# Optimization experiments

Measured on AMD Instinct MI355X. Metric: run time of the kernel, lower is better.

Reference implementation:

```python
import jax, jax.numpy as jnp
import numpy as np

B = 16; Hp = 24; Wp = 24; N = Hp * Wp + 2  # 578 = patches + cls + freq tokens
D = 768; H = 12; HDIM = D // H
BAND = 64; SD = 16  # sd = min(16, max(4, band_dim))
HID = 3072  # int(embed_dim * mlp_ratio)
SCALE = HDIM ** -0.5; CLIP = 10.0
FILM_SCALE = 0.5; SPEC_INIT = 0.02; GATE_INIT = 0.05


def _ln(x, w, b, eps=1e-6):
    m = jnp.mean(x, axis=-1, keepdims=True)
    v = jnp.mean((x - m) ** 2, axis=-1, keepdims=True)
    return (x - m) * jax.lax.rsqrt(v + eps) * w + b


def _rms(x, eps=1e-6):
    return x * jax.lax.rsqrt(jnp.mean(x * x, axis=-1, keepdims=True) + eps)


def setup_inputs() -> dict:
    key = jax.random.key(0)
    ks = jax.random.split(key, 16)
    rn = lambda k, s, sc=1.0: jax.random.normal(k, s, dtype=jnp.float32) * sc
    return {
        "x": rn(ks[0], (B, N, D)),
        "band_tokens": rn(ks[1], (B, 1, D)),  # unused by forward (matches torch signature)
        "freq_token_for_cond": rn(ks[2], (B, 1, D)),
        "freq_summary": rn(ks[3], (B, D)),
        "token_band_feat": rn(ks[4], (B, N, BAND)),
        "alpha": jnp.ones((1,), jnp.float32),
        "ln_gate_w": jnp.ones((D,), jnp.float32), "ln_gate_b": jnp.zeros((D,), jnp.float32),
        "film_w": rn(ks[5], (D, 2 * D), 1e-4), "film_b": jnp.zeros((2 * D,), jnp.float32),
        "ln_attn_w": jnp.ones((D,), jnp.float32), "ln_attn_b": jnp.zeros((D,), jnp.float32),
        "qkv_w": rn(ks[6], (D, 3 * D), 0.02), "qkv_b": jnp.zeros((3 * D,), jnp.float32),
        "proj_w": rn(ks[7], (D, D), 0.02), "proj_b": jnp.zeros((D,), jnp.float32),
        "spec_bias_scale": jnp.float32(SPEC_INIT),
        "gate_w": rn(ks[8], (D, H), 1e-4), "gate_b": jnp.zeros((H,), jnp.float32),
        "band_proj_w": rn(ks[9], (BAND, SD), 0.02),
        "ln_mlp_w": jnp.ones((D,), jnp.float32), "ln_mlp_b": jnp.zeros((D,), jnp.float32),
        "fc1_w": rn(ks[10], (D, HID), 0.02), "fc1_b": jnp.zeros((HID,), jnp.float32),
        "fc2_w": rn(ks[11], (HID, D), 0.02), "fc2_b": jnp.zeros((D,), jnp.float32),
        "dw_w": rn(ks[12], (HID, 1, 3, 3), 0.1), "dw_b": jnp.zeros((HID,), jnp.float32),
    }


def _forward(x, band_tokens, freq_token_for_cond, freq_summary, token_band_feat, alpha,
             ln_gate_w, ln_gate_b, film_w, film_b, ln_attn_w, ln_attn_b,
             qkv_w, qkv_b, proj_w, proj_b, spec_bias_scale, gate_w, gate_b, band_proj_w,
             ln_mlp_w, ln_mlp_b, fc1_w, fc1_b, fc2_w, fc2_b, dw_w, dw_b):
    a = alpha.reshape(())
    # --- FiLM gate on patch tokens (replaces patch, no residual) ---
    cls_freq = x[:, :2]
    patch = x[:, 2:]
    p = _ln(patch, ln_gate_w, ln_gate_b)
    gb = freq_summary @ film_w + film_b            # [B, 2D]
    gamma, beta = jnp.split(gb, 2, axis=-1)
    gamma = jnp.tanh(gamma) * FILM_SCALE
    beta = jnp.tanh(beta) * FILM_SCALE
    patch = p * (1.0 + a * gamma[:, None, :]) + a * beta[:, None, :]
    x = jnp.concatenate([cls_freq, patch], axis=1)
    # --- spectral-similarity attention ---
    xn = _ln(x, ln_attn_w, ln_attn_b)
    qkv = (xn @ qkv_w + qkv_b).reshape(B, N, 3, H, HDIM)
    q = _rms(qkv[:, :, 0].transpose(0, 2, 1, 3))   # [B,H,N,hd]
    k = _rms(qkv[:, :, 1].transpose(0, 2, 1, 3))
    v = qkv[:, :, 2].transpose(0, 2, 1, 3)
    logits = jnp.einsum('bhnd,bhmd->bhnm', q * SCALE, k)
    s = _rms(token_band_feat @ band_proj_w)        # [B,N,SD]
    ssim = jnp.einsum('bns,bms->bnm', s, s)        # [B,N,N]
    logits = jnp.clip(logits + a * spec_bias_scale * ssim[:, None], -CLIP, CLIP)
    attn = jax.nn.softmax(logits, axis=-1)
    out = jnp.einsum('bhnm,bhmd->bhnd', attn, v)
    g = jnp.tanh(freq_token_for_cond[:, 0] @ gate_w + gate_b) * GATE_INIT  # [B,H]
    out = out * (1.0 + a * g[:, :, None, None])
    out = out.transpose(0, 2, 1, 3).reshape(B, N, D)
    x = x + (out @ proj_w + proj_b)
    # --- conv MLP on patch tokens only ---
    cls_freq = x[:, :2]
    patch = x[:, 2:]
    h = jax.nn.gelu(_ln(patch, ln_mlp_w, ln_mlp_b) @ fc1_w + fc1_b, approximate=False)
    h = h.transpose(0, 2, 1).reshape(B, HID, Hp, Wp)
    h = jax.lax.conv_general_dilated(h, dw_w, (1, 1), 'SAME', feature_group_count=HID,
                                     dimension_numbers=('NCHW', 'OIHW', 'NCHW'))
    h = jax.nn.silu(h + dw_b[None, :, None, None])
    h = h.reshape(B, HID, Hp * Wp).transpose(0, 2, 1)
    patch = patch + (h @ fc2_w + fc2_b)
    return jnp.concatenate([cls_freq, patch], axis=1)


def reference(x, band_tokens, freq_token_for_cond, freq_summary, token_band_feat, alpha,
              ln_gate_w, ln_gate_b, film_w, film_b, ln_attn_w, ln_attn_b,
              qkv_w, qkv_b, proj_w, proj_b, spec_bias_scale, gate_w, gate_b, band_proj_w,
              ln_mlp_w, ln_mlp_b, fc1_w, fc1_b, fc2_w, fc2_b, dw_w, dw_b):
    return _forward(x, band_tokens, freq_token_for_cond, freq_summary, token_band_feat, alpha,
                    ln_gate_w, ln_gate_b, film_w, film_b, ln_attn_w, ln_attn_b,
                    qkv_w, qkv_b, proj_w, proj_b, spec_bias_scale, gate_w, gate_b, band_proj_w,
                    ln_mlp_w, ln_mlp_b, fc1_w, fc1_b, fc2_w, fc2_b, dw_w, dw_b)
```

## Files before the change

### kernel.cpp

```cpp
#include <hip/hip_runtime.h>
#include <hip/hip_bf16.h>

#define BATCH 16
#define NTOK 578
#define NTOKP 592
#define NP 576
#define PGRID 24
#define DIM 768
#define NH 12
#define HDIM 64
#define BAND 64
#define SDIM 16
#define HID 3072
#define SCALE 0.125f
#define CLIPV 10.0f
#define KHS 104
#define VTS 72
#define PLS 72

typedef __attribute__((ext_vector_type(8))) short bf16x8;
typedef __attribute__((ext_vector_type(4))) float f32x4;

__device__ __forceinline__ float b2f(short u) {
  union { float f; unsigned int i; } x;
  x.i = ((unsigned int)(unsigned short)u) << 16;
  return x.f;
}
__device__ __forceinline__ short f2b(float x) {
  __hip_bfloat16 h = __float2bfloat16(x);
  return *reinterpret_cast<short*>(&h);
}

__device__ __forceinline__ void gload16(const short* g, short* l) {
  __builtin_amdgcn_global_load_lds(
      (const __attribute__((address_space(1))) unsigned int*)g,
      (__attribute__((address_space(3))) unsigned int*)l, 16, 0, 0);
}

__device__ __forceinline__ int swz_wgid(int orig, int nwg) {
  int xcd = orig & 7, i = orig >> 3;
  int q = nwg >> 3, r = nwg & 7;
  return (xcd < r) ? xcd * (q + 1) + i : r * (q + 1) + (xcd - r) * q + i;
}

__device__ __forceinline__ void block_reduce2(float& a, float& b) {
  __shared__ float sm[8];
  #pragma unroll
  for (int o = 32; o > 0; o >>= 1) { a += __shfl_down(a, o); b += __shfl_down(b, o); }
  int lane = threadIdx.x & 63, w = threadIdx.x >> 6;
  __syncthreads();
  if (lane == 0) { sm[w] = a; sm[4 + w] = b; }
  __syncthreads();
  a = sm[0] + sm[1] + sm[2] + sm[3];
  b = sm[4] + sm[5] + sm[6] + sm[7];
}

__device__ __forceinline__ void tw_body(
    const float* __restrict__ W, short* __restrict__ Wt, int K, int N,
    int kblk, int nblk, float (*t)[33]) {
  int k0 = kblk * 32, n0 = nblk * 32;
  int tx = threadIdx.x & 31, ty = threadIdx.x >> 5;
  #pragma unroll
  for (int i = 0; i < 4; i++)
    t[ty + 8 * i][tx] = W[(size_t)(k0 + ty + 8 * i) * N + n0 + tx];
  __syncthreads();
  #pragma unroll
  for (int i = 0; i < 4; i++)
    Wt[(size_t)(n0 + ty + 8 * i) * K + k0 + tx] = f2b(t[tx][ty + 8 * i]);
}

__global__ __launch_bounds__(256) void prep_weights(
    const float* __restrict__ qkv_w, const float* __restrict__ proj_w,
    const float* __restrict__ fc1_w, const float* __restrict__ fc2_w,
    const float* __restrict__ dww,
    short* __restrict__ qkvT, short* __restrict__ projT,
    short* __restrict__ fc1T, short* __restrict__ fc2T, float* __restrict__ dwt) {
  __shared__ float t[32][33];
  int id = blockIdx.x;
  if (id < 1728) {
    tw_body(qkv_w, qkvT, 768, 2304, id % 24, id / 24, t);
  } else if (id < 2304) {
    int u = id - 1728; tw_body(proj_w, projT, 768, 768, u % 24, u / 24, t);
  } else if (id < 4608) {
    int u = id - 2304; tw_body(fc1_w, fc1T, 768, 3072, u % 24, u / 24, t);
  } else if (id < 6912) {
    int u = id - 4608; tw_body(fc2_w, fc2T, 3072, 768, u % 96, u / 96, t);
  } else {
    int i = (id - 6912) * 256 + threadIdx.x;
    if (i < 9 * HID) { int tt = i / HID, c = i - tt * HID; dwt[i] = dww[c * 9 + tt]; }
  }
}

__global__ __launch_bounds__(256) void transpose_v(
    const short* __restrict__ v, short* __restrict__ vT) {
  __shared__ short t[64][72];
  int bh = blockIdx.y;
  int n0 = blockIdx.x * 64;
  int tid = threadIdx.x;
  const short* vb = v + (size_t)bh * NTOK * HDIM;
  short* ob = vT + (size_t)bh * HDIM * NTOKP;
  {
    int r = tid >> 2, c0 = (tid & 3) * 16;
    int n = n0 + r;
    bf16x8 a0 = {0,0,0,0,0,0,0,0}, a1 = {0,0,0,0,0,0,0,0};
    if (n < NTOK) {
      a0 = *(const bf16x8*)(vb + (size_t)n * HDIM + c0);
      a1 = *(const bf16x8*)(vb + (size_t)n * HDIM + c0 + 8);
    }
    *(bf16x8*)(&t[r][c0]) = a0;
    *(bf16x8*)(&t[r][c0 + 8]) = a1;
  }
  __syncthreads();
  {
    int d = tid & 63, nc = tid >> 6;
    int nbase = n0 + nc * 16;
    short tmp[16];
    #pragma unroll
    for (int e = 0; e < 16; e++) tmp[e] = t[nc * 16 + e][d];
    if (nbase + 16 <= NTOK) {
      *(bf16x8*)(ob + (size_t)d * NTOKP + nbase) = *(bf16x8*)tmp;
      *(bf16x8*)(ob + (size_t)d * NTOKP + nbase + 8) = *(bf16x8*)(tmp + 8);
    } else {
      for (int e = 0; e < 16; e++)
        if (nbase + e < NTOK) ob[(size_t)d * NTOKP + nbase + e] = tmp[e];
    }
  }
}

__global__ __launch_bounds__(256) void film_kernel(
    const float* __restrict__ fsum, const float* __restrict__ film_w, const float* __restrict__ film_b,
    const float* __restrict__ ftc, const float* __restrict__ gate_w, const float* __restrict__ gate_b,
    float* __restrict__ gamma, float* __restrict__ beta, float* __restrict__ g) {
  int bid = blockIdx.x, tid = threadIdx.x;
  if (bid < 24) {
    __shared__ float fs[BATCH][DIM];
    for (int i = tid; i < BATCH * DIM; i += 256) fs[i / DIM][i - (i / DIM) * DIM] = fsum[i];
    __syncthreads();
    int col = bid * 64 + (tid & 63);
    int b0 = tid >> 6;
    float acc[4];
    float bv = film_b[col];
    #pragma unroll
    for (int i = 0; i < 4; i++) acc[i] = bv;
    for (int k = 0; k < DIM; k++) {
      float w = film_w[(size_t)k * 2 * DIM + col];
      #pragma unroll
      for (int i = 0; i < 4; i++) acc[i] += fs[b0 + 4 * i][k] * w;
    }
    #pragma unroll
    for (int i = 0; i < 4; i++) {
      int b = b0 + 4 * i;
      float t = tanhf(acc[i]) * 0.5f;
      if (col < DIM) gamma[b * DIM + col] = t;
      else beta[b * DIM + (col - DIM)] = t;
    }
  } else {
    int i2 = tid;
    if (i2 < BATCH * NH) {
      int b = i2 / NH, h = i2 - b * NH;
      float acc = gate_b[h];
      for (int i = 0; i < DIM; i++) acc += ftc[b * DIM + i] * gate_w[i * NH + h];
      g[i2] = tanhf(acc) * 0.05f;
    }
  }
}

__global__ __launch_bounds__(256) void ln_film_kernel(
    const float* __restrict__ x, const float* __restrict__ gamma, const float* __restrict__ beta,
    const float* __restrict__ gw, const float* __restrict__ gb,
    const float* __restrict__ aw, const float* __restrict__ ab,
    const float* __restrict__ alpha, float* __restrict__ xw, __hip_bfloat16* __restrict__ xn) {
  int row = blockIdx.x;
  int b = row / NTOK, n = row % NTOK;
  int tid = threadIdx.x;
  const float* xr = x + (size_t)row * DIM;
  float vals[3];
  #pragma unroll
  for (int j = 0; j < 3; j++) vals[j] = xr[tid + j * 256];
  if (n >= 2) {
    float s = vals[0] + vals[1] + vals[2];
    float ss = vals[0]*vals[0] + vals[1]*vals[1] + vals[2]*vals[2];
    block_reduce2(s, ss);
    float mean = s * (1.f / 768.f);
    float inv = rsqrtf(ss * (1.f / 768.f) - mean * mean + 1e-6f);
    float a = alpha[0];
    #pragma unroll
    for (int j = 0; j < 3; j++) {
      int d = tid + j * 256;
      float p = (vals[j] - mean) * inv * gw[d] + gb[d];
      vals[j] = p * (1.f + a * gamma[(size_t)b * DIM + d]) + a * beta[(size_t)b * DIM + d];
    }
  }
  float* xwr = xw + (size_t)row * DIM;
  #pragma unroll
  for (int j = 0; j < 3; j++) xwr[tid + j * 256] = vals[j];
  float s = vals[0] + vals[1] + vals[2];
  float ss = vals[0]*vals[0] + vals[1]*vals[1] + vals[2]*vals[2];
  block_reduce2(s, ss);
  float mean = s * (1.f / 768.f);
  float inv = rsqrtf(ss * (1.f / 768.f) - mean * mean + 1e-6f);
  __hip_bfloat16* xnr = xn + (size_t)row * DIM;
  #pragma unroll
  for (int j = 0; j < 3; j++) {
    int d = tid + j * 256;
    xnr[d] = __float2bfloat16((vals[j] - mean) * inv * aw[d] + ab[d]);
  }
}

__global__ __launch_bounds__(256) void band_s_kernel(
    const float* __restrict__ tbf, const float* __restrict__ bw, float* __restrict__ s) {
  int row = blockIdx.x * 4 + (threadIdx.x >> 6);
  int lane = threadIdx.x & 63;
  if (row >= BATCH * NTOK) return;
  const float* t = tbf + (size_t)row * BAND;
  float val = 0.f;
  if (lane < SDIM) {
    for (int i = 0; i < BAND; i++) val += t[i] * bw[i * SDIM + lane];
  }
  float ss = val * val;
  #pragma unroll
  for (int o = 8; o > 0; o >>= 1) ss += __shfl_xor(ss, o, 16);
  if (lane < SDIM) s[(size_t)row * SDIM + lane] = val * rsqrtf(ss * (1.f / 16.f) + 1e-6f);
}

__device__ __forceinline__ void stage_tile256(
    const short* __restrict__ A, const short* __restrict__ Wt, int K,
    int m0, int n0, int kt, short* Al, short* Bl, int wid, int lrow, int lcol) {
  #pragma unroll
  for (int it = 0; it < 4; it++) {
    int r0 = wid * 8 + it * 64;
    gload16(A + (size_t)(m0 + r0 + lrow) * K + kt + lcol, Al + r0 * 64);
  }
  #pragma unroll
  for (int it = 0; it < 2; it++) {
    int r0 = wid * 8 + it * 64;
    gload16(Wt + (size_t)(n0 + r0 + lrow) * K + kt + lcol, Bl + r0 * 64);
  }
}

__device__ __forceinline__ void compute_tile256(
    const short* Al, const short* Bl, f32x4 acc[4][4],
    int wr, int wc, int ln15, int kb) {
  #pragma unroll
  for (int kk = 0; kk < 2; kk++) {
    bf16x8 af[4], bfr[4];
    #pragma unroll
    for (int i = 0; i < 4; i++)
      af[i] = *(const bf16x8*)(Al + (wr * 64 + i * 16 + ln15) * 64 + kk * 32 + kb * 8);
    #pragma unroll
    for (int j = 0; j < 4; j++)
      bfr[j] = *(const bf16x8*)(Bl + (wc * 64 + j * 16 + ln15) * 64 + kk * 32 + kb * 8);
    #pragma unroll
    for (int i = 0; i < 4; i++)
      #pragma unroll
      for (int j = 0; j < 4; j++)
        acc[i][j] = __builtin_amdgcn_mfma_f32_16x16x32_bf16(af[i], bfr[j], acc[i][j], 0, 0, 0);
  }
}

__device__ __forceinline__ void mfma_core_256(
    const short* __restrict__ A, const short* __restrict__ Wt,
    int K, int m0, int n0, f32x4 acc[4][4], short* Al, short* Bl) {
  int tid = threadIdx.x, lane = tid & 63, wid = tid >> 6;
  int wr = wid >> 1, wc = wid & 1;
  int ln15 = lane & 15, kb = lane >> 4;
  int lrow = lane >> 3, lcol = (lane & 7) * 8;
  #pragma unroll
  for (int i = 0; i < 4; i++)
    #pragma unroll
    for (int j = 0; j < 4; j++) acc[i][j] = (f32x4){0.f, 0.f, 0.f, 0.f};
  for (int kt = 0; kt < K; kt += 64) {
    stage_tile256(A, Wt, K, m0, n0, kt, Al, Bl, wid, lrow, lcol);
    __syncthreads();
    compute_tile256(Al, Bl, acc, wr, wc, ln15, kb);
    __syncthreads();
  }
}

__device__ __forceinline__ void stage_tile(
    const short* __restrict__ A, const short* __restrict__ Wt, int K,
    int m0, int n0, int kt, short* Al, short* Bl, int wid, int lrow, int lcol) {
  #pragma unroll
  for (int it = 0; it < 4; it++) {
    int r0 = wid * 8 + it * 32;
    gload16(A + (size_t)(m0 + r0 + lrow) * K + kt + lcol, Al + r0 * 64);
    gload16(Wt + (size_t)(n0 + r0 + lrow) * K + kt + lcol, Bl + r0 * 64);
  }
}

__device__ __forceinline__ void stage_tile64(
    const short* __restrict__ A, const short* __restrict__ Wt, int K,
    int m0, int n0, int kt, short* Al, short* Bl, int wid, int lrow, int lcol) {
  #pragma unroll
  for (int it = 0; it < 2; it++) {
    int r0 = wid * 8 + it * 32;
    gload16(A + (size_t)(m0 + r0 + lrow) * K + kt + lcol, Al + r0 * 64);
  }
  #pragma unroll
  for (int it = 0; it < 4; it++) {
    int r0 = wid * 8 + it * 32;
    gload16(Wt + (size_t)(n0 + r0 + lrow) * K + kt + lcol, Bl + r0 * 64);
  }
}

__device__ __forceinline__ void compute_tile64(
    const short* Al, const short* Bl, f32x4 acc[4][2],
    int wid, int ln15, int kb) {
  #pragma unroll
  for (int kk = 0; kk < 2; kk++) {
    bf16x8 af[4], bfr[2];
    #pragma unroll
    for (int i = 0; i < 4; i++)
      af[i] = *(const bf16x8*)(Al + (i * 16 + ln15) * 64 + kk * 32 + kb * 8);
    #pragma unroll
    for (int j = 0; j < 2; j++)
      bfr[j] = *(const bf16x8*)(Bl + (wid * 32 + j * 16 + ln15) * 64 + kk * 32 + kb * 8);
    #pragma unroll
    for (int i = 0; i < 4; i++)
      #pragma unroll
      for (int j = 0; j < 2; j++)
        acc[i][j] = __builtin_amdgcn_mfma_f32_16x16x32_bf16(af[i], bfr[j], acc[i][j], 0, 0, 0);
  }
}

__device__ __forceinline__ void mfma_core_64(
    const short* __restrict__ A, const short* __restrict__ Wt,
    int K, int m0, int n0, f32x4 acc[4][2],
    short* Al0, short* Bl0, short* Al1, short* Bl1) {
  int tid = threadIdx.x, lane = tid & 63, wid = tid >> 6;
  int ln15 = lane & 15, kb = lane >> 4;
  int lrow = lane >> 3, lcol = (lane & 7) * 8;
  #pragma unroll
  for (int i = 0; i < 4; i++)
    #pragma unroll
    for (int j = 0; j < 2; j++) acc[i][j] = (f32x4){0.f, 0.f, 0.f, 0.f};
  stage_tile64(A, Wt, K, m0, n0, 0, Al0, Bl0, wid, lrow, lcol);
  __syncthreads();
  for (int kt = 0; kt < K; kt += 128) {
    if (kt + 64 < K)
      stage_tile64(A, Wt, K, m0, n0, kt + 64, Al1, Bl1, wid, lrow, lcol);
    compute_tile64(Al0, Bl0, acc, wid, ln15, kb);
    __syncthreads();
    if (kt + 128 < K)
      stage_tile64(A, Wt, K, m0, n0, kt + 128, Al0, Bl0, wid, lrow, lcol);
    if (kt + 64 < K)
      compute_tile64(Al1, Bl1, acc, wid, ln15, kb);
    __syncthreads();
  }
}

__global__ __launch_bounds__(512) void gemm_qkv(
    const short* __restrict__ A, const short* __restrict__ Wt, const float* __restrict__ bias,
    __hip_bfloat16* __restrict__ q, __hip_bfloat16* __restrict__ k, __hip_bfloat16* __restrict__ v) {
  __shared__ short Al[256 * 64], Bl[128 * 64];
  f32x4 acc[4][4];
  int wgid = swz_wgid(blockIdx.x, 37 * 18);
  int m0 = (wgid / 18) * 256, n0 = (wgid % 18) * 128;
  mfma_core_256(A, Wt, DIM, m0, n0, acc, Al, Bl);
  int tid = threadIdx.x, lane = tid & 63, wid = tid >> 6, wr = wid >> 1, wc = wid & 1;
  int ln15 = lane & 15, lq = lane >> 4;
  int colbase = n0 + wc * 64;
  int which = colbase / DIM;
  int rem = colbase - which * DIM;
  int h = rem >> 6;
  __hip_bfloat16* dst = (which == 0) ? q : ((which == 1) ? k : v);
  float fin_scale = (which == 0) ? SCALE : 1.0f;
  float bv[4];
  #pragma unroll
  for (int j = 0; j < 4; j++) bv[j] = bias[colbase + j * 16 + ln15];
  #pragma unroll
  for (int i = 0; i < 4; i++) {
    #pragma unroll
    for (int r = 0; r < 4; r++) {
      int m = m0 + wr * 64 + i * 16 + lq * 4 + r;
      float v4[4];
      #pragma unroll
      for (int j = 0; j < 4; j++) v4[j] = acc[i][j][r] + bv[j];
      float inv = fin_scale;
      if (which < 2) {
        float ss = v4[0]*v4[0] + v4[1]*v4[1] + v4[2]*v4[2] + v4[3]*v4[3];
        ss += __shfl_xor(ss, 1); ss += __shfl_xor(ss, 2);
        ss += __shfl_xor(ss, 4); ss += __shfl_xor(ss, 8);
        inv = rsqrtf(ss * (1.f / 64.f) + 1e-6f) * fin_scale;
      }
      if (m < BATCH * NTOK) {
        int b = m / NTOK, n = m - b * NTOK;
        __hip_bfloat16* orow = dst + (((size_t)b * NH + h) * NTOK + n) * HDIM;
        #pragma unroll
        for (int j = 0; j < 4; j++)
          orow[j * 16 + ln15] = __float2bfloat16(v4[j] * inv);
      }
    }
  }
}

__global__ __launch_bounds__(512) void attn_mfma(
    const short* __restrict__ q, const short* __restrict__ k,
    const short* __restrict__ vT, const float* __restrict__ s,
    const float* __restrict__ g, const float* __restrict__ alpha,
    const float* __restrict__ sbs, short* __restrict__ ao) {
  __shared__ short Kh[2][64 * KHS];
  __shared__ short Vt[2][64 * VTS];
  __shared__ short Pl[8][16 * PLS];
  int xcd = blockIdx.x & 7, idx = blockIdx.x >> 3;
  int bh = xcd * 24 + idx / 5;
  int n0 = (idx % 5) * 128;
  int b = bh / NH, h = bh - b * NH;
  int tid = threadIdx.x, lane = tid & 63, w = tid >> 6;
  int l15 = lane & 15, lg = lane >> 4;
  float a = alpha[0], c = a * sbs[0];
  const short* qb = q + (size_t)bh * NTOK * HDIM;
  const short* kb = k + (size_t)bh * NTOK * HDIM;
  const short* vtb = vT + (size_t)bh * HDIM * NTOKP;
  const float* sb = s + (size_t)b * NTOK * SDIM;
  const bf16x8 Z8 = {0, 0, 0, 0, 0, 0, 0, 0};

  int qrow = n0 + w * 16 + l15;
  int qsrc = (qrow < NTOK) ? qrow : 0;
  bf16x8 qf0 = *(const bf16x8*)(qb + (size_t)qsrc * HDIM + lg * 8);
  bf16x8 qf1 = *(const bf16x8*)(qb + (size_t)qsrc * HDIM + 32 + lg * 8);
  bf16x8 qf2 = Z8;
  if (lg < 2) {
    const float* sp = sb + (size_t)qsrc * SDIM + lg * 8;
    #pragma unroll
    for (int j = 0; j < 8; j++) qf2[j] = f2b(c * sp[j]);
  }

  f32x4 accO[4];
  #pragma unroll
  for (int dd = 0; dd < 4; dd++) accO[dd] = (f32x4){0.f, 0.f, 0.f, 0.f};
  float rsum[4] = {0.f, 0.f, 0.f, 0.f};

  int srow = (tid & 255) >> 2, sseg = tid & 3;
  if (tid < 256 && sseg == 3) {
    #pragma unroll
    for (int bb = 0; bb < 2; bb++) {
      short* dst = Kh[bb] + srow * KHS + 80;
      *(bf16x8*)dst = Z8;
      *(bf16x8*)(dst + 8) = Z8;
    }
  }

  auto stage = [&](int mt, short* KhB, short* VtB) {
// ... 58 lines not shown
      sa[jj] = __builtin_amdgcn_mfma_f32_16x16x32_bf16(qf2, *(const bf16x8*)(kp + 64), sa[jj], 0, 0, 0);
    }
    __builtin_amdgcn_s_setprio(0);
    short* pw = Pl[w];
    float ps[4][4];
    #pragma unroll
    for (int jj = 0; jj < 4; jj++) {
      bool ok = (mt + jj * 16 + l15) < NTOK;
      #pragma unroll
      for (int r = 0; r < 4; r++) {
        float x = sa[jj][r];
        x = fminf(fmaxf(x, -CLIPV), CLIPV);
        float e = ok ? __expf(x) : 0.f;
        ps[jj][r] = e;
        pw[(lg * 4 + r) * PLS + jj * 16 + l15] = f2b(e);
      }
    }
    #pragma unroll
    for (int r = 0; r < 4; r++) {
      float t = ps[0][r] + ps[1][r] + ps[2][r] + ps[3][r];
      t += __shfl_xor(t, 1); t += __shfl_xor(t, 2);
      t += __shfl_xor(t, 4); t += __shfl_xor(t, 8);
      rsum[r] += t;
    }
    __builtin_amdgcn_s_setprio(1);
    #pragma unroll
    for (int kc = 0; kc < 2; kc++) {
      bf16x8 pa = *(const bf16x8*)(pw + l15 * PLS + kc * 32 + lg * 8);
      #pragma unroll
      for (int dd = 0; dd < 4; dd++) {
        bf16x8 vf = *(const bf16x8*)(VtC + (dd * 16 + l15) * VTS + kc * 32 + lg * 8);
        accO[dd] = __builtin_amdgcn_mfma_f32_16x16x32_bf16(pa, vf, accO[dd], 0, 0, 0);
      }
    }
    __builtin_amdgcn_s_setprio(0);
    __syncthreads();
  }
  float gm = 1.f + a * g[bh];
  #pragma unroll
  for (int r = 0; r < 4; r++) {
    int n = n0 + w * 16 + lg * 4 + r;
    if (n >= NTOK) continue;
    float inv = gm / rsum[r];
    short* orow = ao + ((size_t)b * NTOK + n) * DIM + h * HDIM;
    #pragma unroll
    for (int dd = 0; dd < 4; dd++)
      orow[dd * 16 + l15] = f2b(accO[dd][r] * inv);
  }
}

__global__ __launch_bounds__(256) void gemm_proj(
    const short* __restrict__ A, const short* __restrict__ Wt, const float* __restrict__ bias,
    float* __restrict__ xw, float* __restrict__ out) {
  __shared__ short Al[2 * 64 * 64], Bl[2 * 128 * 64];
  f32x4 acc[4][2];
  int wgid = swz_wgid(blockIdx.x, 145 * 6);
  int m0 = (wgid / 6) * 64, n0 = (wgid % 6) * 128;
  mfma_core_64(A, Wt, DIM, m0, n0, acc, Al, Bl, Al + 64 * 64, Bl + 128 * 64);
  int tid = threadIdx.x, lane = tid & 63, wid = tid >> 6;
  int ln15 = lane & 15, lq = lane >> 4;
  #pragma unroll
  for (int i = 0; i < 4; i++) {
    #pragma unroll
    for (int j = 0; j < 2; j++) {
      int col = n0 + wid * 32 + j * 16 + ln15;
      float bv = bias[col];
      #pragma unroll
      for (int r = 0; r < 4; r++) {
        int m = m0 + i * 16 + lq * 4 + r;
        if (m >= BATCH * NTOK) continue;
        int n = m % NTOK;
        float val = acc[i][j][r] + bv + xw[(size_t)m * DIM + col];
        xw[(size_t)m * DIM + col] = val;
        if (n < 2) out[(size_t)m * DIM + col] = val;
      }
    }
  }
}

__global__ __launch_bounds__(256) void ln_mlp_kernel(
    const float* __restrict__ x2, const float* __restrict__ w, const float* __restrict__ bb,
    __hip_bfloat16* __restrict__ xm) {
  int r = blockIdx.x;
  int b = r / NP, pi = r % NP;
  int tid = threadIdx.x;
  const float* xr = x2 + ((size_t)b * NTOK + 2 + pi) * DIM;
  float vals[3];
  #pragma unroll
  for (int j = 0; j < 3; j++) vals[j] = xr[tid + j * 256];
  float s = vals[0] + vals[1] + vals[2];
  float ss = vals[0]*vals[0] + vals[1]*vals[1] + vals[2]*vals[2];
  block_reduce2(s, ss);
  float mean = s * (1.f / 768.f);
  float inv = rsqrtf(ss * (1.f / 768.f) - mean * mean + 1e-6f);
  __hip_bfloat16* xo = xm + (size_t)r * DIM;
  #pragma unroll
  for (int j = 0; j < 3; j++) {
    int d = tid + j * 256;
    xo[d] = __float2bfloat16((vals[j] - mean) * inv * w[d] + bb[d]);
  }
}

__global__ __launch_bounds__(512) void gemm_fc1(
    const short* __restrict__ A, const short* __restrict__ Wt, const float* __restrict__ bias,
    __hip_bfloat16* __restrict__ h1) {
  __shared__ short Al[256 * 64], Bl[128 * 64];
  f32x4 acc[4][4];
  int wgid = swz_wgid(blockIdx.x, 18 * 24);
  int m0 = (wgid / 24) * 256, n0 = (wgid % 24) * 128;
  mfma_core_256(A, Wt, DIM, m0, n0, acc, Al, Bl);
  int tid = threadIdx.x, lane = tid & 63, wid = tid >> 6, wr = wid >> 1, wc = wid & 1;
  int ln15 = lane & 15, lq = lane >> 4;
  #pragma unroll
  for (int i = 0; i < 4; i++) {
    #pragma unroll
    for (int j = 0; j < 4; j++) {
      int col = n0 + wc * 64 + j * 16 + ln15;
      float bv = bias[col];
      #pragma unroll
      for (int r = 0; r < 4; r++) {
        int m = m0 + wr * 64 + i * 16 + lq * 4 + r;
        float val = acc[i][j][r] + bv;
        float ge = 0.5f * val * (1.f + erff(val * 0.70710678118f));
        h1[(size_t)m * HID + col] = __float2bfloat16(ge);
      }
    }
  }
}

__global__ __launch_bounds__(256) void dwconv_kernel(
    const __hip_bfloat16* __restrict__ h1, const float* __restrict__ dwt,
    const float* __restrict__ dwb, __hip_bfloat16* __restrict__ h2) {
  int gx = blockIdx.x;
  int b = gx / 144, g = gx - b * 144;
  int y = g / 6, x0 = (g - y * 6) * 4;
  int tid = threadIdx.x;
  int c0 = blockIdx.y * 512 + (tid & 63) * 8;
  int x = x0 + (tid >> 6);
  const short* in = (const short*)h1 + (size_t)b * NP * HID + c0;
  bf16x8 iv[3][3];
  #pragma unroll
  for (int ky = 0; ky < 3; ky++) {
    int yy = y + ky - 1;
    #pragma unroll
    for (int kx = 0; kx < 3; kx++) {
      int xx = x + kx - 1;
      bool ok = (yy >= 0 && yy < PGRID && xx >= 0 && xx < PGRID);
      iv[ky][kx] = ok ? *(const bf16x8*)(in + (size_t)(yy * PGRID + xx) * HID)
                      : (bf16x8){0, 0, 0, 0, 0, 0, 0, 0};
    }
  }
  float acc[8];
  {
    float4 b0 = *(const float4*)(dwb + c0);
    float4 b1 = *(const float4*)(dwb + c0 + 4);
    acc[0] = b0.x; acc[1] = b0.y; acc[2] = b0.z; acc[3] = b0.w;
    acc[4] = b1.x; acc[5] = b1.y; acc[6] = b1.z; acc[7] = b1.w;
  }
  #pragma unroll
  for (int t = 0; t < 9; t++) {
    float4 w0 = *(const float4*)(dwt + t * HID + c0);
    float4 w1 = *(const float4*)(dwt + t * HID + c0 + 4);
    bf16x8 xv = iv[t / 3][t % 3];
    acc[0] += b2f(xv[0]) * w0.x; acc[1] += b2f(xv[1]) * w0.y;
    acc[2] += b2f(xv[2]) * w0.z; acc[3] += b2f(xv[3]) * w0.w;
    acc[4] += b2f(xv[4]) * w1.x; acc[5] += b2f(xv[5]) * w1.y;
    acc[6] += b2f(xv[6]) * w1.z; acc[7] += b2f(xv[7]) * w1.w;
  }
  short ov[8];
  #pragma unroll
  for (int e = 0; e < 8; e++) {
    float v = acc[e];
    ov[e] = f2b(v / (1.f + __expf(-v)));
  }
  *(bf16x8*)((short*)h2 + ((size_t)b * NP + y * PGRID + x) * HID + c0) = *(bf16x8*)ov;
}

__global__ __launch_bounds__(256) void gemm_fc2(
    const short* __restrict__ A, const short* __restrict__ Wt, const float* __restrict__ bias,
    const float* __restrict__ xw, float* __restrict__ out, int b0) {
  __shared__ short Al[2 * 64 * 64], Bl[2 * 128 * 64];
  f32x4 acc[4][2];
  int wgid = swz_wgid(blockIdx.x, 72 * 6);
  int m0 = (wgid / 6) * 64, n0 = (wgid % 6) * 128;
  mfma_core_64(A, Wt, HID, m0, n0, acc, Al, Bl, Al + 64 * 64, Bl + 128 * 64);
  int tid = threadIdx.x, lane = tid & 63, wid = tid >> 6;
  int ln15 = lane & 15, lq = lane >> 4;
  #pragma unroll
  for (int i = 0; i < 4; i++) {
    #pragma unroll
    for (int j = 0; j < 2; j++) {
      int col = n0 + wid * 32 + j * 16 + ln15;
      float bv = bias[col];
      #pragma unroll
      for (int r = 0; r < 4; r++) {
        int m = m0 + i * 16 + lq * 4 + r;
        int bl = m / NP, pi = m - bl * NP;
        size_t orow = ((size_t)(b0 + bl) * NTOK + 2 + pi) * DIM;
        out[orow + col] = acc[i][j][r] + bv + xw[orow + col];
      }
    }
  }
}

extern "C" void kernel_launch(void* const* d_in, const int* in_sizes, int n_in,
                              void* d_out, int out_size, void* d_ws, size_t ws_size,
                              hipStream_t stream) {
  const float* x      = (const float*)d_in[0];
  const float* ftc    = (const float*)d_in[2];
  const float* fsum   = (const float*)d_in[3];
  const float* tbf    = (const float*)d_in[4];
  const float* alpha  = (const float*)d_in[5];
  const float* lgw    = (const float*)d_in[6];
  const float* lgb    = (const float*)d_in[7];
  const float* film_w = (const float*)d_in[8];
  const float* film_b = (const float*)d_in[9];
  const float* law    = (const float*)d_in[10];
  const float* lab    = (const float*)d_in[11];
  const float* qkv_w  = (const float*)d_in[12];
  const float* qkv_b  = (const float*)d_in[13];
  const float* proj_w = (const float*)d_in[14];
  const float* proj_b = (const float*)d_in[15];
  const float* sbs    = (const float*)d_in[16];
  const float* gate_w = (const float*)d_in[17];
  const float* gate_b = (const float*)d_in[18];
  const float* band_w = (const float*)d_in[19];
  const float* lmw    = (const float*)d_in[20];
  const float* lmb    = (const float*)d_in[21];
  const float* fc1_w  = (const float*)d_in[22];
  const float* fc1_b  = (const float*)d_in[23];
  const float* fc2_w  = (const float*)d_in[24];
  const float* fc2_b  = (const float*)d_in[25];
  const float* dw_w   = (const float*)d_in[26];
  const float* dw_b   = (const float*)d_in[27];
  float* out = (float*)d_out;

  float* ws = (float*)d_ws;
  const size_t SZ = (size_t)BATCH * NTOK * DIM;

  float* p_xw = ws;
  short* p_xn = (short*)(ws + SZ);
  short* p_q  = (short*)(ws + SZ + SZ / 2);
  short* p_k  = (short*)(ws + 2 * SZ);
  short* p_v  = (short*)(ws + 2 * SZ + SZ / 2);
  float* p_s  = ws + 3 * SZ;
  float* p_gamma = p_s + (size_t)BATCH * NTOK * SDIM;
  float* p_beta  = p_gamma + BATCH * DIM;
  float* p_g     = p_beta + BATCH * DIM;
  float* p_dwt   = p_g + 256;
  float* wtb = p_dwt + 9 * HID;
  short* qkvT = (short*)wtb;
  short* projT = qkvT + (size_t)768 * 2304;
  short* fc1T  = projT + (size_t)768 * 768;
  short* fc2T  = fc1T + (size_t)768 * 3072;
  short* h2c   = fc2T + (size_t)3072 * 768;

  const size_t total_floats =
      3 * SZ + (size_t)BATCH * NTOK * SDIM + 2 * (size_t)BATCH * DIM + 256 + 9 * HID +
      ((size_t)768 * 2304 + 768 * 768 + 768 * 3072 + 3072 * 768) / 2 +
      ((size_t)8 * NP * HID) / 2;
  if (ws_size < total_floats * sizeof(float)) return;

  short* p_ao = p_xn;
  short* p_xm = p_q;
  short* h1c  = p_k;
  short* p_vT = h2c;

  dim3 blk(256);

  prep_weights<<<dim3(7020), blk, 0, stream>>>(
      qkv_w, proj_w, fc1_w, fc2_w, dw_w, qkvT, projT, fc1T, fc2T, p_dwt);

  film_kernel<<<dim3(25), blk, 0, stream>>>(
      fsum, film_w, film_b, ftc, gate_w, gate_b, p_gamma, p_beta, p_g);

  ln_film_kernel<<<dim3(BATCH * NTOK), blk, 0, stream>>>(
      x, p_gamma, p_beta, lgw, lgb, law, lab, alpha, p_xw, (__hip_bfloat16*)p_xn);

  band_s_kernel<<<dim3((BATCH * NTOK + 3) / 4), blk, 0, stream>>>(tbf, band_w, p_s);

  gemm_qkv<<<dim3(37 * 18), dim3(512), 0, stream>>>(
      p_xn, qkvT, qkv_b, (__hip_bfloat16*)p_q, (__hip_bfloat16*)p_k, (__hip_bfloat16*)p_v);

  transpose_v<<<dim3(10, BATCH * NH), blk, 0, stream>>>(p_v, p_vT);

  attn_mfma<<<dim3(960), dim3(512), 0, stream>>>(
      p_q, p_k, p_vT, p_s, p_g, alpha, sbs, p_ao);

  gemm_proj<<<dim3(145 * 6), blk, 0, stream>>>(p_ao, projT, proj_b, p_xw, out);

  ln_mlp_kernel<<<dim3(BATCH * NP), blk, 0, stream>>>(p_xw, lmw, lmb, (__hip_bfloat16*)p_xm);

  for (int cc = 0; cc < 2; cc++) {
    const short* Ach = p_xm + (size_t)cc * 4608 * DIM;
    gemm_fc1<<<dim3(18 * 24), dim3(512), 0, stream>>>(Ach, fc1T, fc1_b, (__hip_bfloat16*)h1c);
    dwconv_kernel<<<dim3(8 * 144, 6), blk, 0, stream>>>(
        (const __hip_bfloat16*)h1c, p_dwt, dw_b, (__hip_bfloat16*)h2c);
    gemm_fc2<<<dim3(72 * 6), blk, 0, stream>>>(h2c, fc2T, fc2_b, p_xw, out, cc * 8);
  }
}
```

Before: 517.3 us.

## Double-buffer GEMM LDS staging and write V transposed from QKV GEMM

Replaces the single-buffered and ping-pong GEMM main loops with a two-stage prefetch pipeline. The loop uses explicit vmcnt waits and raw s_barrier, so global loads for tile t+2 overlap the MFMA work on tile t. The QKV GEMM epilogue now writes V directly into the transposed vT layout, which removes the separate transpose kernel and its extra round trip through memory. In exchange, LDS use for the 256-row GEMMs doubles, which may lower occupancy. The vT stores are strided single-element writes that may coalesce poorly.

```diff
diff --git a/kernel.cpp b/kernel.cpp
--- a/kernel.cpp
+++ b/kernel.cpp
@@ -91,42 +91,6 @@
   }
 }
 
-__global__ __launch_bounds__(256) void transpose_v(
-    const short* __restrict__ v, short* __restrict__ vT) {
-  __shared__ short t[64][72];
-  int bh = blockIdx.y;
-  int n0 = blockIdx.x * 64;
-  int tid = threadIdx.x;
-  const short* vb = v + (size_t)bh * NTOK * HDIM;
-  short* ob = vT + (size_t)bh * HDIM * NTOKP;
-  {
-    int r = tid >> 2, c0 = (tid & 3) * 16;
-    int n = n0 + r;
-    bf16x8 a0 = {0,0,0,0,0,0,0,0}, a1 = {0,0,0,0,0,0,0,0};
-    if (n < NTOK) {
-      a0 = *(const bf16x8*)(vb + (size_t)n * HDIM + c0);
-      a1 = *(const bf16x8*)(vb + (size_t)n * HDIM + c0 + 8);
-    }
-    *(bf16x8*)(&t[r][c0]) = a0;
-    *(bf16x8*)(&t[r][c0 + 8]) = a1;
-  }
-  __syncthreads();
-  {
-    int d = tid & 63, nc = tid >> 6;
-    int nbase = n0 + nc * 16;
-    short tmp[16];
-    #pragma unroll
-    for (int e = 0; e < 16; e++) tmp[e] = t[nc * 16 + e][d];
-    if (nbase + 16 <= NTOK) {
-      *(bf16x8*)(ob + (size_t)d * NTOKP + nbase) = *(bf16x8*)tmp;
-      *(bf16x8*)(ob + (size_t)d * NTOKP + nbase + 8) = *(bf16x8*)(tmp + 8);
-    } else {
-      for (int e = 0; e < 16; e++)
-        if (nbase + e < NTOK) ob[(size_t)d * NTOKP + nbase + e] = tmp[e];
-    }
-  }
-}
-
 __global__ __launch_bounds__(256) void film_kernel(
     const float* __restrict__ fsum, const float* __restrict__ film_w, const float* __restrict__ film_b,
     const float* __restrict__ ftc, const float* __restrict__ gate_w, const float* __restrict__ gate_b,
@@ -223,7 +187,7 @@
   if (lane < SDIM) s[(size_t)row * SDIM + lane] = val * rsqrtf(ss * (1.f / 16.f) + 1e-6f);
 }
 
-__device__ __forceinline__ void stage_tile256(
+__device__ __forceinline__ void stage256(
     const short* __restrict__ A, const short* __restrict__ Wt, int K,
     int m0, int n0, int kt, short* Al, short* Bl, int wid, int lrow, int lcol) {
   #pragma unroll
@@ -238,7 +202,7 @@
   }
 }
 
-__device__ __forceinline__ void compute_tile256(
+__device__ __forceinline__ void compute256(
     const short* Al, const short* Bl, f32x4 acc[4][4],
     int wr, int wc, int ln15, int kb) {
   #pragma unroll
@@ -258,9 +222,10 @@
   }
 }
 
-__device__ __forceinline__ void mfma_core_256(
+__device__ __forceinline__ void core256c(
     const short* __restrict__ A, const short* __restrict__ Wt,
-    int K, int m0, int n0, f32x4 acc[4][4], short* Al, short* Bl) {
+    int K, int m0, int n0, f32x4 acc[4][4],
+    short* Al0, short* Bl0, short* Al1, short* Bl1) {
   int tid = threadIdx.x, lane = tid & 63, wid = tid >> 6;
   int wr = wid >> 1, wc = wid & 1;
   int ln15 = lane & 15, kb = lane >> 4;
@@ -269,26 +234,29 @@
   for (int i = 0; i < 4; i++)
     #pragma unroll
     for (int j = 0; j < 4; j++) acc[i][j] = (f32x4){0.f, 0.f, 0.f, 0.f};
-  for (int kt = 0; kt < K; kt += 64) {
-    stage_tile256(A, Wt, K, m0, n0, kt, Al, Bl, wid, lrow, lcol);
-    __syncthreads();
-    compute_tile256(Al, Bl, acc, wr, wc, ln15, kb);
-    __syncthreads();
-  }
-}
-
-__device__ __forceinline__ void stage_tile(
-    const short* __restrict__ A, const short* __restrict__ Wt, int K,
-    int m0, int n0, int kt, short* Al, short* Bl, int wid, int lrow, int lcol) {
-  #pragma unroll
-  for (int it = 0; it < 4; it++) {
-    int r0 = wid * 8 + it * 32;
-    gload16(A + (size_t)(m0 + r0 + lrow) * K + kt + lcol, Al + r0 * 64);
-    gload16(Wt + (size_t)(n0 + r0 + lrow) * K + kt + lcol, Bl + r0 * 64);
-  }
-}
-
-__device__ __forceinline__ void stage_tile64(
+  stage256(A, Wt, K, m0, n0, 0, Al0, Bl0, wid, lrow, lcol);
+  stage256(A, Wt, K, m0, n0, 64, Al1, Bl1, wid, lrow, lcol);
+  asm volatile("s_waitcnt vmcnt(6)" ::: "memory");
+  __builtin_amdgcn_s_barrier();
+  const int NKT = K >> 6;
+  for (int t = 0; t < NKT; t++) {
+    const short* Ac = (t & 1) ? Al1 : Al0;
+    const short* Bc = (t & 1) ? Bl1 : Bl0;
+    compute256(Ac, Bc, acc, wr, wc, ln15, kb);
+    __builtin_amdgcn_s_barrier();
+    if (t + 2 < NKT) {
+      short* As = (t & 1) ? Al1 : Al0;
+      short* Bs = (t & 1) ? Bl1 : Bl0;
+      stage256(A, Wt, K, m0, n0, (t + 2) << 6, As, Bs, wid, lrow, lcol);
+      asm volatile("s_waitcnt vmcnt(6)" ::: "memory");
+    } else {
+      asm volatile("s_waitcnt vmcnt(0)" ::: "memory");
+    }
+    __builtin_amdgcn_s_barrier();
+  }
+}
+
+__device__ __forceinline__ void stage64(
     const short* __restrict__ A, const short* __restrict__ Wt, int K,
     int m0, int n0, int kt, short* Al, short* Bl, int wid, int lrow, int lcol) {
   #pragma unroll
@@ -303,7 +271,7 @@
   }
 }
 
-__device__ __forceinline__ void compute_tile64(
+__device__ __forceinline__ void compute64(
     const short* Al, const short* Bl, f32x4 acc[4][2],
     int wid, int ln15, int kb) {
   #pragma unroll
@@ -323,7 +291,7 @@
   }
 }
 
-__device__ __forceinline__ void mfma_core_64(
+__device__ __forceinline__ void core64c(
     const short* __restrict__ A, const short* __restrict__ Wt,
     int K, int m0, int n0, f32x4 acc[4][2],
     short* Al0, short* Bl0, short* Al1, short* Bl1) {
@@ -334,36 +302,42 @@
   for (int i = 0; i < 4; i++)
     #pragma unroll
     for (int j = 0; j < 2; j++) acc[i][j] = (f32x4){0.f, 0.f, 0.f, 0.f};
-  stage_tile64(A, Wt, K, m0, n0, 0, Al0, Bl0, wid, lrow, lcol);
-  __syncthreads();
-  for (int kt = 0; kt < K; kt += 128) {
-    if (kt + 64 < K)
-      stage_tile64(A, Wt, K, m0, n0, kt + 64, Al1, Bl1, wid, lrow, lcol);
-    compute_tile64(Al0, Bl0, acc, wid, ln15, kb);
-    __syncthreads();
-    if (kt + 128 < K)
-      stage_tile64(A, Wt, K, m0, n0, kt + 128, Al0, Bl0, wid, lrow, lcol);
-    if (kt + 64 < K)
-      compute_tile64(Al1, Bl1, acc, wid, ln15, kb);
-    __syncthreads();
+  stage64(A, Wt, K, m0, n0, 0, Al0, Bl0, wid, lrow, lcol);
+  stage64(A, Wt, K, m0, n0, 64, Al1, Bl1, wid, lrow, lcol);
+  asm volatile("s_waitcnt vmcnt(6)" ::: "memory");
+  __builtin_amdgcn_s_barrier();
+  const int NKT = K >> 6;
+  for (int t = 0; t < NKT; t++) {
+    const short* Ac = (t & 1) ? Al1 : Al0;
+    const short* Bc = (t & 1) ? Bl1 : Bl0;
+    compute64(Ac, Bc, acc, wid, ln15, kb);
+    __builtin_amdgcn_s_barrier();
+    if (t + 2 < NKT) {
+      short* As = (t & 1) ? Al1 : Al0;
+      short* Bs = (t & 1) ? Bl1 : Bl0;
+      stage64(A, Wt, K, m0, n0, (t + 2) << 6, As, Bs, wid, lrow, lcol);
+      asm volatile("s_waitcnt vmcnt(6)" ::: "memory");
+    } else {
+      asm volatile("s_waitcnt vmcnt(0)" ::: "memory");
+    }
+    __builtin_amdgcn_s_barrier();
   }
 }
 
 __global__ __launch_bounds__(512) void gemm_qkv(
     const short* __restrict__ A, const short* __restrict__ Wt, const float* __restrict__ bias,
-    __hip_bfloat16* __restrict__ q, __hip_bfloat16* __restrict__ k, __hip_bfloat16* __restrict__ v) {
-  __shared__ short Al[256 * 64], Bl[128 * 64];
+    __hip_bfloat16* __restrict__ q, __hip_bfloat16* __restrict__ k, short* __restrict__ vT) {
+  __shared__ short Al0[256 * 64], Bl0[128 * 64], Al1[256 * 64], Bl1[128 * 64];
   f32x4 acc[4][4];
   int wgid = swz_wgid(blockIdx.x, 37 * 18);
   int m0 = (wgid / 18) * 256, n0 = (wgid % 18) * 128;
-  mfma_core_256(A, Wt, DIM, m0, n0, acc, Al, Bl);
+  core256c(A, Wt, DIM, m0, n0, acc, Al0, Bl0, Al1, Bl1);
   int tid = threadIdx.x, lane = tid & 63, wid = tid >> 6, wr = wid >> 1, wc = wid & 1;
   int ln15 = lane & 15, lq = lane >> 4;
   int colbase = n0 + wc * 64;
   int which = colbase / DIM;
   int rem = colbase - which * DIM;
   int h = rem >> 6;
-  __hip_bfloat16* dst = (which == 0) ? q : ((which == 1) ? k : v);
   float fin_scale = (which == 0) ? SCALE : 1.0f;
   float bv[4];
   #pragma unroll
@@ -385,10 +359,18 @@
       }
       if (m < BATCH * NTOK) {
         int b = m / NTOK, n = m - b * NTOK;
-        __hip_bfloat16* orow = dst + (((size_t)b * NH + h) * NTOK + n) * HDIM;
-        #pragma unroll
-        for (int j = 0; j < 4; j++)
-          orow[j * 16 + ln15] = __float2bfloat16(v4[j] * inv);
+        if (which == 2) {
+          short* vr = vT + (((size_t)b * NH + h) * HDIM) * NTOKP + n;
+          #pragma unroll
+          for (int j = 0; j < 4; j++)
+            vr[(size_t)(j * 16 + ln15) * NTOKP] = f2b(v4[j]);
+        } else {
+          __hip_bfloat16* dst = (which == 0) ? q : k;
+          __hip_bfloat16* orow = dst + (((size_t)b * NH + h) * NTOK + n) * HDIM;
+          #pragma unroll
+          for (int j = 0; j < 4; j++)
+            orow[j * 16 + ln15] = __float2bfloat16(v4[j] * inv);
+        }
       }
     }
   }
@@ -553,11 +535,11 @@
 __global__ __launch_bounds__(256) void gemm_proj(
     const short* __restrict__ A, const short* __restrict__ Wt, const float* __restrict__ bias,
     float* __restrict__ xw, float* __restrict__ out) {
-  __shared__ short Al[2 * 64 * 64], Bl[2 * 128 * 64];
+  __shared__ short Al0[64 * 64], Bl0[128 * 64], Al1[64 * 64], Bl1[128 * 64];
   f32x4 acc[4][2];
   int wgid = swz_wgid(blockIdx.x, 145 * 6);
   int m0 = (wgid / 6) * 64, n0 = (wgid % 6) * 128;
-  mfma_core_64(A, Wt, DIM, m0, n0, acc, Al, Bl, Al + 64 * 64, Bl + 128 * 64);
+  core64c(A, Wt, DIM, m0, n0, acc, Al0, Bl0, Al1, Bl1);
   int tid = threadIdx.x, lane = tid & 63, wid = tid >> 6;
   int ln15 = lane & 15, lq = lane >> 4;
   #pragma unroll
@@ -605,11 +587,11 @@
 __global__ __launch_bounds__(512) void gemm_fc1(
     const short* __restrict__ A, const short* __restrict__ Wt, const float* __restrict__ bias,
     __hip_bfloat16* __restrict__ h1) {
-  __shared__ short Al[256 * 64], Bl[128 * 64];
+  __shared__ short Al0[256 * 64], Bl0[128 * 64], Al1[256 * 64], Bl1[128 * 64];
   f32x4 acc[4][4];
   int wgid = swz_wgid(blockIdx.x, 18 * 24);
   int m0 = (wgid / 24) * 256, n0 = (wgid % 24) * 128;
-  mfma_core_256(A, Wt, DIM, m0, n0, acc, Al, Bl);
+  core256c(A, Wt, DIM, m0, n0, acc, Al0, Bl0, Al1, Bl1);
   int tid = threadIdx.x, lane = tid & 63, wid = tid >> 6, wr = wid >> 1, wc = wid & 1;
   int ln15 = lane & 15, lq = lane >> 4;
   #pragma unroll
@@ -680,11 +662,11 @@
 __global__ __launch_bounds__(256) void gemm_fc2(
     const short* __restrict__ A, const short* __restrict__ Wt, const float* __restrict__ bias,
     const float* __restrict__ xw, float* __restrict__ out, int b0) {
-  __shared__ short Al[2 * 64 * 64], Bl[2 * 128 * 64];
+  __shared__ short Al0[64 * 64], Bl0[128 * 64], Al1[64 * 64], Bl1[128 * 64];
   f32x4 acc[4][2];
   int wgid = swz_wgid(blockIdx.x, 72 * 6);
   int m0 = (wgid / 6) * 64, n0 = (wgid % 6) * 128;
-  mfma_core_64(A, Wt, HID, m0, n0, acc, Al, Bl, Al + 64 * 64, Bl + 128 * 64);
+  core64c(A, Wt, HID, m0, n0, acc, Al0, Bl0, Al1, Bl1);
   int tid = threadIdx.x, lane = tid & 63, wid = tid >> 6;
   int ln15 = lane & 15, lq = lane >> 4;
   #pragma unroll
@@ -781,9 +763,7 @@
   band_s_kernel<<<dim3((BATCH * NTOK + 3) / 4), blk, 0, stream>>>(tbf, band_w, p_s);
 
   gemm_qkv<<<dim3(37 * 18), dim3(512), 0, stream>>>(
-      p_xn, qkvT, qkv_b, (__hip_bfloat16*)p_q, (__hip_bfloat16*)p_k, (__hip_bfloat16*)p_v);
-
-  transpose_v<<<dim3(10, BATCH * NH), blk, 0, stream>>>(p_v, p_vT);
+      p_xn, qkvT, qkv_b, (__hip_bfloat16*)p_q, (__hip_bfloat16*)p_k, p_vT);
 
   attn_mfma<<<dim3(960), dim3(512), 0, stream>>>(
       p_q, p_k, p_vT, p_s, p_g, alpha, sbs, p_ao);
```

Measured after the change: 573.5 us. 1.11x slower.

## Merge prep, FiLM and band kernels into one launch and reorder GEMM tile mapping

Applied to the files above, without the earlier changes.

Folds the weight-transpose prep, FiLM/gate projection and band RMS projection into a single mega-kernel to cut launch count and let the small jobs overlap the large transpose. It also swaps the workgroup-to-tile mapping in the qkv, proj, fc1 and fc2 GEMMs to column-major order, so neighbouring workgroups share a weight tile instead of an activation row tile, which should change L2 reuse. The mega-kernel now reserves 48KB of shared memory for every block, which may lower occupancy in the transpose blocks.

```diff
diff --git a/kernel.cpp b/kernel.cpp
--- a/kernel.cpp
+++ b/kernel.cpp
@@ -69,25 +69,74 @@
     Wt[(size_t)(n0 + ty + 8 * i) * K + k0 + tx] = f2b(t[tx][ty + 8 * i]);
 }
 
-__global__ __launch_bounds__(256) void prep_weights(
+__global__ __launch_bounds__(256) void prep_mega(
     const float* __restrict__ qkv_w, const float* __restrict__ proj_w,
     const float* __restrict__ fc1_w, const float* __restrict__ fc2_w,
     const float* __restrict__ dww,
+    const float* __restrict__ fsum, const float* __restrict__ film_w,
+    const float* __restrict__ film_b, const float* __restrict__ ftc,
+    const float* __restrict__ gate_w, const float* __restrict__ gate_b,
+    const float* __restrict__ tbf, const float* __restrict__ band_w,
     short* __restrict__ qkvT, short* __restrict__ projT,
-    short* __restrict__ fc1T, short* __restrict__ fc2T, float* __restrict__ dwt) {
-  __shared__ float t[32][33];
-  int id = blockIdx.x;
+    short* __restrict__ fc1T, short* __restrict__ fc2T, float* __restrict__ dwt,
+    float* __restrict__ gamma, float* __restrict__ beta, float* __restrict__ g,
+    float* __restrict__ s) {
+  __shared__ float smem[BATCH * DIM];
+  int id = blockIdx.x, tid = threadIdx.x;
   if (id < 1728) {
-    tw_body(qkv_w, qkvT, 768, 2304, id % 24, id / 24, t);
+    tw_body(qkv_w, qkvT, 768, 2304, id % 24, id / 24, (float(*)[33])smem);
   } else if (id < 2304) {
-    int u = id - 1728; tw_body(proj_w, projT, 768, 768, u % 24, u / 24, t);
+    int u = id - 1728; tw_body(proj_w, projT, 768, 768, u % 24, u / 24, (float(*)[33])smem);
   } else if (id < 4608) {
-    int u = id - 2304; tw_body(fc1_w, fc1T, 768, 3072, u % 24, u / 24, t);
+    int u = id - 2304; tw_body(fc1_w, fc1T, 768, 3072, u % 24, u / 24, (float(*)[33])smem);
   } else if (id < 6912) {
-    int u = id - 4608; tw_body(fc2_w, fc2T, 3072, 768, u % 96, u / 96, t);
+    int u = id - 4608; tw_body(fc2_w, fc2T, 3072, 768, u % 96, u / 96, (float(*)[33])smem);
+  } else if (id < 7020) {
+    int i = (id - 6912) * 256 + tid;
+    if (i < 9 * HID) { int tt = i / HID, c = i - tt * HID; dwt[i] = dww[c * 9 + tt]; }
+  } else if (id < 7044) {
+    float (*fs)[DIM] = (float(*)[DIM])smem;
+    for (int i = tid; i < BATCH * DIM; i += 256) fs[i / DIM][i - (i / DIM) * DIM] = fsum[i];
+    __syncthreads();
+    int col = (id - 7020) * 64 + (tid & 63);
+    int b0 = tid >> 6;
+    float acc[4];
+    float bv = film_b[col];
+    #pragma unroll
+    for (int i = 0; i < 4; i++) acc[i] = bv;
+    for (int k = 0; k < DIM; k++) {
+      float w = film_w[(size_t)k * 2 * DIM + col];
+      #pragma unroll
+      for (int i = 0; i < 4; i++) acc[i] += fs[b0 + 4 * i][k] * w;
+    }
+    #pragma unroll
+    for (int i = 0; i < 4; i++) {
+      int b = b0 + 4 * i;
+      float t = tanhf(acc[i]) * 0.5f;
+      if (col < DIM) gamma[b * DIM + col] = t;
+      else beta[b * DIM + (col - DIM)] = t;
+    }
+  } else if (id == 7044) {
+    if (tid < BATCH * NH) {
+      int b = tid / NH, h = tid - b * NH;
+      float acc = gate_b[h];
+      for (int i = 0; i < DIM; i++) acc += ftc[b * DIM + i] * gate_w[i * NH + h];
+      g[tid] = tanhf(acc) * 0.05f;
+    }
   } else {
-    int i = (id - 6912) * 256 + threadIdx.x;
-    if (i < 9 * HID) { int tt = i / HID, c = i - tt * HID; dwt[i] = dww[c * 9 + tt]; }
+    int row = (id - 7045) * 4 + (tid >> 6);
+    int lane = tid & 63;
+    if (row < BATCH * NTOK) {
+      const float* t = tbf + (size_t)row * BAND;
+      float val = 0.f;
+      if (lane < SDIM) {
+        for (int i = 0; i < BAND; i++) val += t[i] * band_w[i * SDIM + lane];
+      }
+      float ss = val * val;
+      #pragma unroll
+      for (int o = 8; o > 0; o >>= 1) ss += __shfl_xor(ss, o, 16);
+      if (lane < SDIM) s[(size_t)row * SDIM + lane] = val * rsqrtf(ss * (1.f / 16.f) + 1e-6f);
+    }
   }
 }
 
@@ -127,44 +176,6 @@
   }
 }
 
-__global__ __launch_bounds__(256) void film_kernel(
-    const float* __restrict__ fsum, const float* __restrict__ film_w, const float* __restrict__ film_b,
-    const float* __restrict__ ftc, const float* __restrict__ gate_w, const float* __restrict__ gate_b,
-    float* __restrict__ gamma, float* __restrict__ beta, float* __restrict__ g) {
-  int bid = blockIdx.x, tid = threadIdx.x;
-  if (bid < 24) {
-    __shared__ float fs[BATCH][DIM];
-    for (int i = tid; i < BATCH * DIM; i += 256) fs[i / DIM][i - (i / DIM) * DIM] = fsum[i];
-    __syncthreads();
-    int col = bid * 64 + (tid & 63);
-    int b0 = tid >> 6;
-    float acc[4];
-    float bv = film_b[col];
-    #pragma unroll
-    for (int i = 0; i < 4; i++) acc[i] = bv;
-    for (int k = 0; k < DIM; k++) {
-      float w = film_w[(size_t)k * 2 * DIM + col];
-      #pragma unroll
-      for (int i = 0; i < 4; i++) acc[i] += fs[b0 + 4 * i][k] * w;
-    }
-    #pragma unroll
-    for (int i = 0; i < 4; i++) {
-      int b = b0 + 4 * i;
-      float t = tanhf(acc[i]) * 0.5f;
-      if (col < DIM) gamma[b * DIM + col] = t;
-      else beta[b * DIM + (col - DIM)] = t;
-    }
-  } else {
-    int i2 = tid;
-    if (i2 < BATCH * NH) {
-      int b = i2 / NH, h = i2 - b * NH;
-      float acc = gate_b[h];
-      for (int i = 0; i < DIM; i++) acc += ftc[b * DIM + i] * gate_w[i * NH + h];
-      g[i2] = tanhf(acc) * 0.05f;
-    }
-  }
-}
-
 __global__ __launch_bounds__(256) void ln_film_kernel(
     const float* __restrict__ x, const float* __restrict__ gamma, const float* __restrict__ beta,
     const float* __restrict__ gw, const float* __restrict__ gb,
@@ -207,22 +218,6 @@
   }
 }
 
-__global__ __launch_bounds__(256) void band_s_kernel(
-    const float* __restrict__ tbf, const float* __restrict__ bw, float* __restrict__ s) {
-  int row = blockIdx.x * 4 + (threadIdx.x >> 6);
-  int lane = threadIdx.x & 63;
-  if (row >= BATCH * NTOK) return;
-  const float* t = tbf + (size_t)row * BAND;
-  float val = 0.f;
-  if (lane < SDIM) {
-    for (int i = 0; i < BAND; i++) val += t[i] * bw[i * SDIM + lane];
-  }
-  float ss = val * val;
-  #pragma unroll
-  for (int o = 8; o > 0; o >>= 1) ss += __shfl_xor(ss, o, 16);
-  if (lane < SDIM) s[(size_t)row * SDIM + lane] = val * rsqrtf(ss * (1.f / 16.f) + 1e-6f);
-}
-
 __device__ __forceinline__ void stage_tile256(
     const short* __restrict__ A, const short* __restrict__ Wt, int K,
     int m0, int n0, int kt, short* Al, short* Bl, int wid, int lrow, int lcol) {
@@ -274,17 +269,6 @@
     __syncthreads();
     compute_tile256(Al, Bl, acc, wr, wc, ln15, kb);
     __syncthreads();
-  }
-}
-
-__device__ __forceinline__ void stage_tile(
-    const short* __restrict__ A, const short* __restrict__ Wt, int K,
-    int m0, int n0, int kt, short* Al, short* Bl, int wid, int lrow, int lcol) {
-  #pragma unroll
-  for (int it = 0; it < 4; it++) {
-    int r0 = wid * 8 + it * 32;
-    gload16(A + (size_t)(m0 + r0 + lrow) * K + kt + lcol, Al + r0 * 64);
-    gload16(Wt + (size_t)(n0 + r0 + lrow) * K + kt + lcol, Bl + r0 * 64);
   }
 }
 
@@ -355,7 +339,7 @@
   __shared__ short Al[256 * 64], Bl[128 * 64];
   f32x4 acc[4][4];
   int wgid = swz_wgid(blockIdx.x, 37 * 18);
-  int m0 = (wgid / 18) * 256, n0 = (wgid % 18) * 128;
+  int m0 = (wgid % 37) * 256, n0 = (wgid / 37) * 128;
   mfma_core_256(A, Wt, DIM, m0, n0, acc, Al, Bl);
   int tid = threadIdx.x, lane = tid & 63, wid = tid >> 6, wr = wid >> 1, wc = wid & 1;
   int ln15 = lane & 15, lq = lane >> 4;
@@ -553,11 +537,11 @@
 __global__ __launch_bounds__(256) void gemm_proj(
     const short* __restrict__ A, const short* __restrict__ Wt, const float* __restrict__ bias,
     float* __restrict__ xw, float* __restrict__ out) {
-  __shared__ short Al[2 * 64 * 64], Bl[2 * 128 * 64];
+  __shared__ short Al0[64 * 64], Bl0[128 * 64], Al1[64 * 64], Bl1[128 * 64];
   f32x4 acc[4][2];
   int wgid = swz_wgid(blockIdx.x, 145 * 6);
-  int m0 = (wgid / 6) * 64, n0 = (wgid % 6) * 128;
-  mfma_core_64(A, Wt, DIM, m0, n0, acc, Al, Bl, Al + 64 * 64, Bl + 128 * 64);
+  int m0 = (wgid % 145) * 64, n0 = (wgid / 145) * 128;
+  mfma_core_64(A, Wt, DIM, m0, n0, acc, Al0, Bl0, Al1, Bl1);
   int tid = threadIdx.x, lane = tid & 63, wid = tid >> 6;
   int ln15 = lane & 15, lq = lane >> 4;
   #pragma unroll
@@ -608,7 +592,7 @@
   __shared__ short Al[256 * 64], Bl[128 * 64];
   f32x4 acc[4][4];
   int wgid = swz_wgid(blockIdx.x, 18 * 24);
-  int m0 = (wgid / 24) * 256, n0 = (wgid % 24) * 128;
+  int m0 = (wgid % 18) * 256, n0 = (wgid / 18) * 128;
   mfma_core_256(A, Wt, DIM, m0, n0, acc, Al, Bl);
   int tid = threadIdx.x, lane = tid & 63, wid = tid >> 6, wr = wid >> 1, wc = wid & 1;
   int ln15 = lane & 15, lq = lane >> 4;
@@ -680,11 +664,11 @@
 __global__ __launch_bounds__(256) void gemm_fc2(
     const short* __restrict__ A, const short* __restrict__ Wt, const float* __restrict__ bias,
     const float* __restrict__ xw, float* __restrict__ out, int b0) {
-  __shared__ short Al[2 * 64 * 64], Bl[2 * 128 * 64];
+  __shared__ short Al0[64 * 64], Bl0[128 * 64], Al1[64 * 64], Bl1[128 * 64];
   f32x4 acc[4][2];
   int wgid = swz_wgid(blockIdx.x, 72 * 6);
-  int m0 = (wgid / 6) * 64, n0 = (wgid % 6) * 128;
-  mfma_core_64(A, Wt, HID, m0, n0, acc, Al, Bl, Al + 64 * 64, Bl + 128 * 64);
+  int m0 = (wgid % 72) * 64, n0 = (wgid / 72) * 128;
+  mfma_core_64(A, Wt, HID, m0, n0, acc, Al0, Bl0, Al1, Bl1);
   int tid = threadIdx.x, lane = tid & 63, wid = tid >> 6;
   int ln15 = lane & 15, lq = lane >> 4;
   #pragma unroll
@@ -769,16 +753,13 @@
 
   dim3 blk(256);
 
-  prep_weights<<<dim3(7020), blk, 0, stream>>>(
-      qkv_w, proj_w, fc1_w, fc2_w, dw_w, qkvT, projT, fc1T, fc2T, p_dwt);
-
-  film_kernel<<<dim3(25), blk, 0, stream>>>(
-      fsum, film_w, film_b, ftc, gate_w, gate_b, p_gamma, p_beta, p_g);
+  prep_mega<<<dim3(7045 + (BATCH * NTOK + 3) / 4), blk, 0, stream>>>(
+      qkv_w, proj_w, fc1_w, fc2_w, dw_w,
+      fsum, film_w, film_b, ftc, gate_w, gate_b, tbf, band_w,
+      qkvT, projT, fc1T, fc2T, p_dwt, p_gamma, p_beta, p_g, p_s);
 
   ln_film_kernel<<<dim3(BATCH * NTOK), blk, 0, stream>>>(
       x, p_gamma, p_beta, lgw, lgb, law, lab, alpha, p_xw, (__hip_bfloat16*)p_xn);
-
-  band_s_kernel<<<dim3((BATCH * NTOK + 3) / 4), blk, 0, stream>>>(tbf, band_w, p_s);
 
   gemm_qkv<<<dim3(37 * 18), dim3(512), 0, stream>>>(
       p_xn, qkvT, qkv_b, (__hip_bfloat16*)p_q, (__hip_bfloat16*)p_k, (__hip_bfloat16*)p_v);
```

New measurement: 513.6 us. About the same (-0.7%).
